# Kernel optimization log

Hardware: AMD Instinct MI355X
Metric: run time of the kernel (lower is better)

## Reference

```python
import jax, jax.numpy as jnp
import numpy as np

NODE_NUMS = 128
IN_SIZE = 256
OUT_SIZE = 256
BATCH = 4096


def setup_inputs() -> dict:
    key = jax.random.key(0)
    k1, k2, k3, k4, k5 = jax.random.split(key, 5)
    # Xavier-uniform bounds
    limit_w = float(np.sqrt(6.0 / (IN_SIZE + OUT_SIZE)))
    limit_b = float(np.sqrt(6.0 / (NODE_NUMS + OUT_SIZE)))
    x = jax.random.normal(k1, (BATCH, IN_SIZE), dtype=jnp.float32)
    var_vector = jax.random.normal(k2, (BATCH, 16), dtype=jnp.float32)  # unused in forward
    W_1 = jax.random.uniform(k3, (NODE_NUMS, IN_SIZE, OUT_SIZE), dtype=jnp.float32,
                             minval=-limit_w, maxval=limit_w)
    b_1 = jax.random.uniform(k4, (NODE_NUMS, OUT_SIZE), dtype=jnp.float32,
                             minval=-limit_b, maxval=limit_b)
    node_ind = jax.random.randint(k5, (2, BATCH), 0, NODE_NUMS, dtype=jnp.int32)
    return {"x": x, "var_vector": var_vector, "W_1": W_1, "b_1": b_1, "node_ind": node_ind}


def reference(x, var_vector, W_1, b_1, node_ind):
    # idx selects a per-sample expert (node) weight matrix and bias.
    idx = node_ind[1]                       # [B]
    W = W_1[idx]                            # [B, in, out] gathered weights
    b = b_1[idx]                            # [B, out]
    # bmm(x[:,None,:], W).squeeze() + b  ==  einsum over the input dim
    return jnp.einsum('bi,bio->bo', x, W) + b
```

## Files before the change

kernel.cpp:

```cpp
#include <hip/hip_runtime.h>

#define BATCH 4096
#define INS   256
#define OUTS  256
#define NODES 128
#define NT    64
#define MCH   16
#define MSPLIT 2
#define MRANGE (BATCH / MSPLIT)

typedef short short8 __attribute__((ext_vector_type(8)));
typedef float f32x4  __attribute__((ext_vector_type(4)));

struct SMem {
    unsigned short list[MRANGE];
    int cnt;
};

__device__ __forceinline__ unsigned short f2bf(float f) {
    unsigned int u = __builtin_bit_cast(unsigned int, f);
    u += 0x7fffu + ((u >> 16) & 1u);
    return (unsigned short)(u >> 16);
}

__device__ __forceinline__ short8 pack8(float4 a, float4 b) {
    short8 r;
    r[0] = (short)f2bf(a.x); r[1] = (short)f2bf(a.y);
    r[2] = (short)f2bf(a.z); r[3] = (short)f2bf(a.w);
    r[4] = (short)f2bf(b.x); r[5] = (short)f2bf(b.y);
    r[6] = (short)f2bf(b.z); r[7] = (short)f2bf(b.w);
    return r;
}

__global__ __launch_bounds__(256, 4) void moe_fwd(
    const float* __restrict__ x, const float* __restrict__ W1,
    const float* __restrict__ b1, const int* __restrict__ nid,
    float* __restrict__ out)
{
    __shared__ SMem sm;
    const int t   = threadIdx.x;
    const int bid = blockIdx.x;
    const int sub = bid >> 3;
    const int e   = (bid & 7) * 16 + (sub >> 3);
    const int c0  = ((sub >> 1) & 3) * NT;
    const int mh  = sub & 1;

    const int w  = t >> 6;
    const int l  = t & 63;
    const int g  = l >> 4;
    const int ln = l & 15;
    const int cc = c0 + w * 16 + ln;

    if (t == 0) sm.cnt = 0;
    __syncthreads();

    const float* __restrict__ wp = W1 + (size_t)e * (INS * OUTS) + cc;
    short8 wf[8];
    #pragma unroll
    for (int ks = 0; ks < 8; ++ks) {
        short8 v;
        #pragma unroll
        for (int j = 0; j < 8; ++j)
            v[j] = (short)f2bf(wp[(size_t)(ks * 32 + g * 8 + j) * OUTS]);
        wf[ks] = v;
    }
    const float bval = b1[e * OUTS + cc];

    const int* __restrict__ idxp = nid + BATCH + mh * MRANGE;
    #pragma unroll
    for (int it = 0; it < MRANGE / 256; ++it) {
        int b = it * 256 + t;
        if (idxp[b] == e) {
            int p = atomicAdd(&sm.cnt, 1);
            sm.list[p] = (unsigned short)(mh * MRANGE + b);
        }
    }
    asm volatile("s_waitcnt lgkmcnt(0)" ::: "memory");
    __builtin_amdgcn_s_barrier();
    asm volatile("" ::: "memory");

    const int cnt = sm.cnt;
    if (cnt == 0) return;

    for (int m0 = 0; m0 < cnt; m0 += MCH) {
        int r0 = m0 + ln;
        int s0 = sm.list[r0 < cnt ? r0 : cnt - 1];
        const float* __restrict__ xp0 = x + (size_t)s0 * INS + g * 8;

        f32x4 acc0 = {0.f, 0.f, 0.f, 0.f};
        #pragma unroll
        for (int ks = 0; ks < 8; ++ks) {
            float4 u0 = *reinterpret_cast<const float4*>(xp0 + ks * 32);
            float4 u1 = *reinterpret_cast<const float4*>(xp0 + ks * 32 + 4);
            short8 a0 = pack8(u0, u1);
            acc0 = __builtin_amdgcn_mfma_f32_16x16x32_bf16(a0, wf[ks], acc0, 0, 0, 0);
        }

        #pragma unroll
        for (int q = 0; q < 4; ++q) {
            int rr = m0 + g * 4 + q;
            if (rr < cnt)
                out[(size_t)sm.list[rr] * OUTS + cc] = acc0[q] + bval;
        }
    }
}

extern "C" void kernel_launch(void* const* d_in, const int* in_sizes, int n_in,
                              void* d_out, int out_size, void* d_ws, size_t ws_size,
                              hipStream_t stream) {
    const float* x   = (const float*)d_in[0];
    const float* W1  = (const float*)d_in[2];
    const float* b1  = (const float*)d_in[3];
    const int*   nid = (const int*)d_in[4];
    float* out = (float*)d_out;

    hipLaunchKernelGGL(moe_fwd, dim3(NODES * (OUTS / NT) * MSPLIT), dim3(256),
                       0, stream, x, W1, b1, nid, out);
}
```

Measured before the change: 24.38 us.

## Precompute per-expert token lists in a separate scan kernel with global atomics

Moves the per-block routing scan, where every block read 2048 indices and built an LDS list, into a separate scan kernel. That kernel bins tokens per expert into a global workspace using atomics. The GEMM kernel then reads the per-expert count and list and splits the tokens evenly between the two halves, which balances the work better. In exchange it adds a memset and an extra kernel launch with a serial dependency, and it caps each expert's list at 512 tokens. Token order in each list also becomes nondeterministic.

```diff
diff --git a/kernel.cpp b/kernel.cpp
--- a/kernel.cpp
+++ b/kernel.cpp
@@ -7,15 +7,10 @@
 #define NT    64
 #define MCH   16
 #define MSPLIT 2
-#define MRANGE (BATCH / MSPLIT)
+#define MAXC  512
 
 typedef short short8 __attribute__((ext_vector_type(8)));
 typedef float f32x4  __attribute__((ext_vector_type(4)));
-
-struct SMem {
-    unsigned short list[MRANGE];
-    int cnt;
-};
 
 __device__ __forceinline__ unsigned short f2bf(float f) {
     unsigned int u = __builtin_bit_cast(unsigned int, f);
@@ -32,12 +27,21 @@
     return r;
 }
 
+__global__ __launch_bounds__(256) void moe_scan(
+    const int* __restrict__ nid, int* __restrict__ gcnt,
+    unsigned short* __restrict__ glist)
+{
+    int s = blockIdx.x * 256 + threadIdx.x;
+    int e = nid[BATCH + s];
+    int p = atomicAdd(&gcnt[e], 1);
+    if (p < MAXC) glist[e * MAXC + p] = (unsigned short)s;
+}
+
 __global__ __launch_bounds__(256, 4) void moe_fwd(
     const float* __restrict__ x, const float* __restrict__ W1,
-    const float* __restrict__ b1, const int* __restrict__ nid,
-    float* __restrict__ out)
+    const float* __restrict__ b1, float* __restrict__ out,
+    const int* __restrict__ gcnt, const unsigned short* __restrict__ glist)
 {
-    __shared__ SMem sm;
     const int t   = threadIdx.x;
     const int bid = blockIdx.x;
     const int sub = bid >> 3;
@@ -51,8 +55,10 @@
     const int ln = l & 15;
     const int cc = c0 + w * 16 + ln;
 
-    if (t == 0) sm.cnt = 0;
-    __syncthreads();
+    const int cnt  = gcnt[e];
+    const int half = (cnt + 1) >> 1;
+    const int lo   = mh * half;
+    const int hi   = (cnt < lo + half) ? cnt : lo + half;
 
     const float* __restrict__ wp = W1 + (size_t)e * (INS * OUTS) + cc;
     short8 wf[8];
@@ -66,25 +72,13 @@
     }
     const float bval = b1[e * OUTS + cc];
 
-    const int* __restrict__ idxp = nid + BATCH + mh * MRANGE;
-    #pragma unroll
-    for (int it = 0; it < MRANGE / 256; ++it) {
-        int b = it * 256 + t;
-        if (idxp[b] == e) {
-            int p = atomicAdd(&sm.cnt, 1);
-            sm.list[p] = (unsigned short)(mh * MRANGE + b);
-        }
-    }
-    asm volatile("s_waitcnt lgkmcnt(0)" ::: "memory");
-    __builtin_amdgcn_s_barrier();
-    asm volatile("" ::: "memory");
+    if (lo >= hi) return;
 
-    const int cnt = sm.cnt;
-    if (cnt == 0) return;
+    const unsigned short* __restrict__ lst = glist + e * MAXC;
 
-    for (int m0 = 0; m0 < cnt; m0 += MCH) {
+    for (int m0 = lo; m0 < hi; m0 += MCH) {
         int r0 = m0 + ln;
-        int s0 = sm.list[r0 < cnt ? r0 : cnt - 1];
+        int s0 = lst[r0 < hi ? r0 : hi - 1];
         const float* __restrict__ xp0 = x + (size_t)s0 * INS + g * 8;
 
         f32x4 acc0 = {0.f, 0.f, 0.f, 0.f};
@@ -99,8 +93,8 @@
         #pragma unroll
         for (int q = 0; q < 4; ++q) {
             int rr = m0 + g * 4 + q;
-            if (rr < cnt)
-                out[(size_t)sm.list[rr] * OUTS + cc] = acc0[q] + bval;
+            if (rr < hi)
+                out[(size_t)lst[rr] * OUTS + cc] = acc0[q] + bval;
         }
     }
 }
@@ -114,6 +108,12 @@
     const int*   nid = (const int*)d_in[4];
     float* out = (float*)d_out;
 
+    int* gcnt = (int*)d_ws;
+    unsigned short* glist = (unsigned short*)((char*)d_ws + 512);
+
+    hipMemsetAsync(gcnt, 0, NODES * sizeof(int), stream);
+    hipLaunchKernelGGL(moe_scan, dim3(BATCH / 256), dim3(256), 0, stream,
+                       nid, gcnt, glist);
     hipLaunchKernelGGL(moe_fwd, dim3(NODES * (OUTS / NT) * MSPLIT), dim3(256),
-                       0, stream, x, W1, b1, nid, out);
+                       0, stream, x, W1, b1, out, gcnt, glist);
 }
```

Result: slower. 32.42 us (+33.0%).
